# Kernel tuning notes

Measured on AMD Instinct MI355X. Metric: run time of the kernel, lower is better.

The kernel has to match this reference:

```python
import jax, jax.numpy as jnp
import numpy as np

B, S, DIM, HD = 4, 1024, 2048, 128
H = DIM // HD  # 16 heads
GN_EPS = 1e-3  # Keras GroupNormalization default epsilon


def setup_inputs() -> dict:
    key = jax.random.key(0)
    ks = jax.random.split(key, 8)
    x = jax.random.normal(ks[0], (B, S, DIM), dtype=jnp.float32)
    k = jax.random.normal(ks[1], (B, S, DIM), dtype=jnp.float32)
    v = jax.random.normal(ks[2], (B, S, DIM), dtype=jnp.float32)
    # One shared QKV projection weight per head (dict.fromkeys bug in source
    # makes Q, K, V use the SAME Dense layer). Keras Dense: y = x @ W, W:(in,out)
    Wh = jax.random.normal(ks[3], (H, HD, HD), dtype=jnp.float32) / np.sqrt(HD)
    wg_w = jax.random.normal(ks[4], (DIM, DIM), dtype=jnp.float32) / np.sqrt(DIM)
    wo_w = jax.random.normal(ks[5], (DIM, DIM), dtype=jnp.float32) / np.sqrt(DIM)
    gn_gamma = jnp.ones((DIM,), dtype=jnp.float32)
    gn_beta = jnp.zeros((DIM,), dtype=jnp.float32)
    return {"x": x, "k": k, "v": v, "Wh": Wh, "wg_w": wg_w, "wo_w": wo_w,
            "gn_gamma": gn_gamma, "gn_beta": gn_beta}


def _decay_masks(n_heads, seq_len):
    # Source: band_part(gamma**(i-j), 0, -1) then transpose ->
    # D[h, i, j] = gamma_h ** (j - i) for j <= i, else 0.
    gam = 1.0 - 2.0 ** (-5.0 - jnp.arange(n_heads, dtype=jnp.float32))  # (H,)
    idx = jnp.arange(seq_len, dtype=jnp.float32)
    expo = idx[None, :] - idx[:, None]               # (S,S): j - i
    D = jnp.where(expo[None, :, :] <= 0,
                  gam[:, None, None] ** expo[None, :, :], 0.0)  # (H,S,S)
    # TF: D /= reduce_sum(D, 1)**0.5 broadcasts row-sums along the COLUMN axis
    return D / jnp.sqrt(D.sum(axis=-1))[:, None, :]


def reference(x, k, v, Wh, wg_w, wo_w, gn_gamma, gn_beta):
    b, s, dim = x.shape
    h, hd, _ = Wh.shape
    # split last axis into contiguous per-head chunks
    xh = x.reshape(b, s, h, hd)
    kh = k.reshape(b, s, h, hd)
    vh = v.reshape(b, s, h, hd)
    # Q, K, V share the same per-head weight (faithful to dict.fromkeys)
    Q = jnp.einsum('bshd,hde->bshe', xh, Wh)
    K = jnp.einsum('bshd,hde->bshe', kh, Wh)
    V = jnp.einsum('bshd,hde->bshe', vh, Wh)
    scores = jnp.einsum('bshe,bthe->bhst', Q, K) / jnp.sqrt(jnp.float32(hd))
    Dn = _decay_masks(h, s)                          # (H,S,S)
    masked = scores * Dn[None, :, :, :]              # (B,H,S,S)
    # source reduces over axis 0 == BATCH, then abs, then clamp at 1
    A = jnp.maximum(jnp.abs(masked.sum(axis=0)), 1.0)  # (H,S,S)
    O = jnp.einsum('hst,bthe->bshe', A, V).reshape(b, s, dim)
    # GroupNormalization(groups=1): per-token layernorm over channels
    mu = O.mean(axis=-1, keepdims=True)
    var = O.var(axis=-1, keepdims=True)
    Y = (O - mu) / jnp.sqrt(var + GN_EPS) * gn_gamma + gn_beta
    W = jax.nn.relu(x @ wg_w)                        # gated branch
    return (W * Y) @ wo_w
```

## Files before the change

### kernel.cpp

```cpp
#include <hip/hip_runtime.h>
#include <math.h>

constexpr int Bc = 4, Sc = 1024, Dc = 2048, HDc = 128, Hc = 16;
constexpr int BSc = Bc * Sc;
constexpr int KQKc = Bc * HDc;
#define GN_EPS 1e-3f

typedef __bf16 bf16x8 __attribute__((ext_vector_type(8)));
typedef __bf16 bf16x4 __attribute__((ext_vector_type(4)));
typedef float f32x4 __attribute__((ext_vector_type(4)));

constexpr size_t OFF_Q   = 0;
constexpr size_t OFF_K   = OFF_Q + (size_t)Hc * Sc * KQKc / 2;
constexpr size_t OFF_VB  = OFF_K + (size_t)Hc * Sc * KQKc / 2;
constexpr size_t OFF_VT  = OFF_VB + (size_t)BSc * Dc / 2;
constexpr size_t OFF_A   = OFF_VT + (size_t)BSc * Dc / 2;
constexpr size_t OFF_O   = OFF_A + (size_t)Hc * Sc * Sc / 2;
constexpr size_t OFF_CT  = OFF_O + (size_t)BSc * Dc;
constexpr size_t OFF_PN  = OFF_CT + (size_t)Hc * Sc;
constexpr size_t OFF_XB  = OFF_PN + (size_t)Hc * Sc;
constexpr size_t OFF_WGT = OFF_XB + (size_t)BSc * Dc / 2;
constexpr size_t OFF_WOT = OFF_WGT + (size_t)Dc * Dc / 2;
constexpr size_t OFF_SUF = OFF_WOT + (size_t)Dc * Dc / 2;
constexpr size_t OFF_T   = OFF_SUF + (size_t)64 * 9 * HDc;
constexpr size_t OFF_WHT = OFF_T + (size_t)64 * 8 * HDc;
constexpr size_t OFF_KB2 = OFF_A;
constexpr size_t OFF_VB2 = OFF_A + (size_t)BSc * Dc / 2;

#define GLOAD_LDS16(gp, lp)                                               \
  __builtin_amdgcn_global_load_lds(                                       \
      (const __attribute__((address_space(1))) void*)(gp),                \
      (__attribute__((address_space(3))) void*)(lp), 16, 0, 0)


__global__ __launch_bounds__(256) void k_tables(float* __restrict__ ct,
                                                float* __restrict__ pn) {
  int idx = blockIdx.x * 256 + threadIdx.x;
  int h = idx >> 10, t = idx & 1023;
  double gamma = 1.0 - exp2(-(double)(5 + h));
  double l2g = log2(gamma);
  double r = 1.0 / gamma;
  double rowsum = (exp2(-(double)(t + 1) * l2g) - 1.0) / (r - 1.0);
  ct[idx] = (float)(exp2((double)t * l2g) / sqrt(rowsum));
  pn[idx] = (float)exp2(-(double)t * l2g);
}

__global__ __launch_bounds__(256) void k_cast8(const float* __restrict__ src,
                                               __bf16* __restrict__ dst) {
  size_t i = ((size_t)blockIdx.x * 256 + threadIdx.x) * 8;
  float4 a = *(const float4*)(src + i);
  float4 b = *(const float4*)(src + i + 4);
  bf16x8 o;
  o[0] = (__bf16)a.x; o[1] = (__bf16)a.y; o[2] = (__bf16)a.z; o[3] = (__bf16)a.w;
  o[4] = (__bf16)b.x; o[5] = (__bf16)b.y; o[6] = (__bf16)b.z; o[7] = (__bf16)b.w;
  *(bf16x8*)(dst + i) = o;
}

__global__ __launch_bounds__(256) void k_castT(const float* __restrict__ src,
                                               __bf16* __restrict__ dst) {
  __shared__ float t[32][33];
  const int bx = blockIdx.x, by = blockIdx.y;
  const int tid = threadIdx.x;
  const int lx = tid & 31, ly = tid >> 5;
  #pragma unroll
  for (int r = 0; r < 32; r += 8)
    t[ly + r][lx] = src[(size_t)(by * 32 + ly + r) * Dc + bx * 32 + lx];
  __syncthreads();
  #pragma unroll
  for (int r = 0; r < 32; r += 8)
    dst[(size_t)(bx * 32 + ly + r) * Dc + by * 32 + lx] = (__bf16)t[lx][ly + r];
}

__global__ __launch_bounds__(256) void k_whT(const float* __restrict__ Wh,
                                             __bf16* __restrict__ WhT) {
  __shared__ float t[32][33];
  const int h = blockIdx.z;
  const int d0 = blockIdx.x * 32, e0 = blockIdx.y * 32;
  const int tid = threadIdx.x;
  const int lx = tid & 31, ly = tid >> 5;
  #pragma unroll
  for (int r = 0; r < 32; r += 8)
    t[ly + r][lx] = Wh[(size_t)h * HDc * HDc + (d0 + ly + r) * HDc + e0 + lx];
  __syncthreads();
  #pragma unroll
  for (int r = 0; r < 32; r += 8)
    WhT[(size_t)h * HDc * HDc + (e0 + ly + r) * HDc + d0 + lx] =
        (__bf16)t[lx][ly + r];
}

__global__ __launch_bounds__(512) void k_projm(const __bf16* __restrict__ Xb,
                                               const __bf16* __restrict__ Kb2,
                                               const __bf16* __restrict__ Vb2,
                                               const __bf16* __restrict__ WhT,
                                               __bf16* __restrict__ Qo,
                                               __bf16* __restrict__ Ko,
                                               __bf16* __restrict__ Vo) {
  const int r0 = blockIdx.x * 128;
  const int h = blockIdx.y;
  const int z = blockIdx.z;
  const __bf16* src = (z == 0) ? Xb : (z == 1) ? Kb2 : Vb2;
  __shared__ __bf16 As[128 * 32];
  __shared__ __bf16 Bs[128 * 32];
  const int tid = threadIdx.x;
  const int wave = tid >> 6, lane = tid & 63;
  const int wm = (wave >> 2) * 64, wn = (wave & 3) * 32;
  const int grow = wave * 16 + (lane >> 2);
  const int gkb = ((lane & 3) ^ ((lane >> 3) & 3)) * 8;
  const int rl = lane & 15, kq = lane >> 4;
  const int sw8 = (kq ^ ((rl >> 1) & 3)) * 8;
  const int cha = wm >> 4, chb = wn >> 4;
  const __bf16* wb = WhT + (size_t)h * HDc * HDc;
  f32x4 acc[4][2] = {{}};
  for (int k0 = 0; k0 < HDc; k0 += 32) {
    GLOAD_LDS16(src + (size_t)(r0 + grow) * Dc + h * HDc + k0 + gkb,
                As + wave * 512);
    GLOAD_LDS16(wb + (size_t)grow * HDc + k0 + gkb, Bs + wave * 512);
    __syncthreads();
    bf16x8 a[4], b[2];
    #pragma unroll
    for (int i = 0; i < 4; ++i)
      a[i] = *(const bf16x8*)&As[(cha + i) * 512 + rl * 32 + sw8];
    #pragma unroll
    for (int j = 0; j < 2; ++j)
      b[j] = *(const bf16x8*)&Bs[(chb + j) * 512 + rl * 32 + sw8];
    #pragma unroll
    for (int i = 0; i < 4; ++i)
      #pragma unroll
      for (int j = 0; j < 2; ++j)
        acc[i][j] = __builtin_amdgcn_mfma_f32_16x16x32_bf16(a[i], b[j],
                                                            acc[i][j], 0, 0, 0);
    __syncthreads();
  }
  #pragma unroll
  for (int i = 0; i < 4; ++i) {
    #pragma unroll
    for (int j = 0; j < 2; ++j) {
      const int col = wn + j * 16 + rl;
      #pragma unroll
      for (int r = 0; r < 4; ++r) {
        const int row = r0 + wm + i * 16 + kq * 4 + r;
        const __bf16 v = (__bf16)acc[i][j][r];
        if (z == 2) {
          Vo[(size_t)row * Dc + h * HDc + col] = v;
        } else {
          const int s = row & 1023, bb = row >> 10;
          __bf16* dst = (z == 0) ? Qo : Ko;
          dst[((size_t)(h * Sc + s) * Bc + bb) * HDc + col] = v;
        }
      }
    }
  }
}

__global__ __launch_bounds__(256) void k_vt(const __bf16* __restrict__ VB,
                                            __bf16* __restrict__ Vt) {
  __shared__ float tl[32][33];
  const int bh = blockIdx.z, bb = bh >> 4, h = bh & 15;
  const int t0 = blockIdx.x * 32, e0 = blockIdx.y * 32;
  const int tid = threadIdx.x;
  const int lx = tid & 31, ly = tid >> 5;
  #pragma unroll
  for (int r = 0; r < 32; r += 8)
    tl[ly + r][lx] =
        (float)VB[(size_t)(bb * Sc + t0 + ly + r) * Dc + h * HDc + e0 + lx];
  __syncthreads();
  #pragma unroll
  for (int r = 0; r < 32; r += 8)
    Vt[((size_t)bh * HDc + e0 + ly + r) * Sc + t0 + lx] = (__bf16)tl[lx][ly + r];
}

__global__ __launch_bounds__(256) void k_vsum(const __bf16* __restrict__ VB,
                                              float* __restrict__ T) {
  const int jj = blockIdx.x, bh = blockIdx.y;
  const int bb = bh >> 4, h = bh & 15;
  const int tid = threadIdx.x;
  const int tp = tid >> 7, e = tid & 127;
  const __bf16* base =
      VB + (size_t)(bb * Sc + jj * 128 + tp * 64) * Dc + h * HDc + e;
  float a0 = 0.f, a1 = 0.f, a2 = 0.f, a3 = 0.f;
  float a4 = 0.f, a5 = 0.f, a6 = 0.f, a7 = 0.f;
  for (int t = 0; t < 64; t += 8) {
    a0 += (float)base[(size_t)(t + 0) * Dc];
    a1 += (float)base[(size_t)(t + 1) * Dc];
    a2 += (float)base[(size_t)(t + 2) * Dc];
    a3 += (float)base[(size_t)(t + 3) * Dc];
    a4 += (float)base[(size_t)(t + 4) * Dc];
    a5 += (float)base[(size_t)(t + 5) * Dc];
    a6 += (float)base[(size_t)(t + 6) * Dc];
    a7 += (float)base[(size_t)(t + 7) * Dc];
  }
  const float s = ((a0 + a1) + (a2 + a3)) + ((a4 + a5) + (a6 + a7));
  __shared__ float red[2][128];
  red[tp][e] = s;
  __syncthreads();
  if (tp == 0)
    T[((size_t)bh * 8 + jj) * HDc + e] = red[0][e] + red[1][e];
}

__global__ __launch_bounds__(128) void k_vscan(const float* __restrict__ T,
                                               float* __restrict__ SufV) {
  const int bh = blockIdx.x;
  const int e = threadIdx.x;
  float acc = 0.f;
  SufV[((size_t)bh * 9 + 8) * HDc + e] = 0.f;
  for (int jj = 7; jj >= 1; --jj) {
    acc += T[((size_t)bh * 8 + jj) * HDc + e];
    SufV[((size_t)bh * 9 + jj) * HDc + e] = acc;
  }
}

__global__ __launch_bounds__(512) void k_ssm(const __bf16* __restrict__ Q,
                                             const __bf16* __restrict__ Kb,
                                             const float* __restrict__ ct,
                                             const float* __restrict__ pn,
                                             __bf16* __restrict__ A) {
  const int bx = blockIdx.x, by = blockIdx.y;
  if (bx > by) return;
  const int h = blockIdx.z;
  const int t0 = bx * 128, s0 = by * 128;
  const int tid = threadIdx.x;
  __bf16* Ah = A + (size_t)h * Sc * Sc;
  __shared__ __bf16 Qs[128 * 32];
  __shared__ __bf16 Ks[128 * 32];
  const int wave = tid >> 6, lane = tid & 63;
  const int wm = (wave >> 2) * 64, wn = (wave & 3) * 32;
  const int grow = wave * 16 + (lane >> 2);
  const int gkb = ((lane & 3) ^ ((lane >> 3) & 3)) * 8;
  const int rl = lane & 15, kq = lane >> 4;
  const int sw8 = (kq ^ ((rl >> 1) & 3)) * 8;
  const int cha = wm >> 4, chb = wn >> 4;
  f32x4 acc[4][2] = {{}};
  const __bf16* qbase = Q + (size_t)(h * Sc + s0) * KQKc;
  const __bf16* kbase = Kb + (size_t)(h * Sc + t0) * KQKc;
  for (int k0 = 0; k0 < KQKc; k0 += 32) {
    GLOAD_LDS16(qbase + (size_t)grow * KQKc + k0 + gkb, Qs + wave * 512);
    GLOAD_LDS16(kbase + (size_t)grow * KQKc + k0 + gkb, Ks + wave * 512);
    __syncthreads();
    bf16x8 a[4], b[2];
    #pragma unroll
    for (int i = 0; i < 4; ++i)
      a[i] = *(const bf16x8*)&Qs[(cha + i) * 512 + rl * 32 + sw8];
    #pragma unroll
    for (int j = 0; j < 2; ++j)
      b[j] = *(const bf16x8*)&Ks[(chb + j) * 512 + rl * 32 + sw8];
    #pragma unroll
    for (int i = 0; i < 4; ++i)
      #pragma unroll
      for (int j = 0; j < 2; ++j)
        acc[i][j] = __builtin_amdgcn_mfma_f32_16x16x32_bf16(a[i], b[j],
                                                            acc[i][j], 0, 0, 0);
    __syncthreads();
  }
  const float rs = 0.088388347648318447f;
  #pragma unroll
  for (int i = 0; i < 4; ++i) {
    #pragma unroll
    for (int j = 0; j < 2; ++j) {
      const int t = t0 + wn + j * 16 + rl;
      const float ctv = ct[h * Sc + t] * rs;
      #pragma unroll
      for (int r = 0; r < 4; ++r) {
        const int s = s0 + wm + i * 16 + kq * 4 + r;
        float v = 1.0f;
        if (t <= s) v = fmaxf(fabsf(ctv * pn[h * Sc + s] * acc[i][j][r]), 1.0f);
        Ah[(size_t)s * Sc + t] = (__bf16)v;
      }
    }
  }
}

__global__ __launch_bounds__(512) void k_avm(const __bf16* __restrict__ A,
                                             const __bf16* __restrict__ Vt,
                                             const float* __restrict__ SufV,
                                             float* __restrict__ O) {
  const int bh = blockIdx.z, bb = bh >> 4, h = bh & 15;
  const int itile = blockIdx.x;
  const int s0 = itile * 128;
  const int tid = threadIdx.x;
  __shared__ __bf16 As[128 * 32];
  __shared__ __bf16 Bs[128 * 32];
  const int wave = tid >> 6, lane = tid & 63;
  const int wm = (wave >> 2) * 64, wn = (wave & 3) * 32;
  const int grow = wave * 16 + (lane >> 2);
  const int gkb = ((lane & 3) ^ ((lane >> 3) & 3)) * 8;
  const int rl = lane & 15, kq = lane >> 4;
  const int sw8 = (kq ^ ((rl >> 1) & 3)) * 8;
  const int cha = wm >> 4, chb = wn >> 4;
  f32x4 acc[4][2] = {{}};
  const __bf16* abase = A + (size_t)(h * Sc + s0) * Sc;
  const __bf16* vbase = Vt + (size_t)bh * HDc * Sc;
  const int kmax = (itile + 1) * 128;
  for (int k0 = 0; k0 < kmax; k0 += 32) {
    GLOAD_LDS16(abase + (size_t)grow * Sc + k0 + gkb, As + wave * 512);
    GLOAD_LDS16(vbase + (size_t)grow * Sc + k0 + gkb, Bs + wave * 512);
    __syncthreads();
    bf16x8 a[4], b[2];
    #pragma unroll
    for (int i = 0; i < 4; ++i)
      a[i] = *(const bf16x8*)&As[(cha + i) * 512 + rl * 32 + sw8];
    #pragma unroll
    for (int j = 0; j < 2; ++j)
      b[j] = *(const bf16x8*)&Bs[(chb + j) * 512 + rl * 32 + sw8];
    #pragma unroll
    for (int i = 0; i < 4; ++i)
      #pragma unroll
      for (int j = 0; j < 2; ++j)
        acc[i][j] = __builtin_amdgcn_mfma_f32_16x16x32_bf16(a[i], b[j],
                                                            acc[i][j], 0, 0, 0);
    __syncthreads();
  }
  const float* sufr = SufV + ((size_t)bh * 9 + (itile + 1)) * HDc;
  #pragma unroll
  for (int i = 0; i < 4; ++i) {
    #pragma unroll
    for (int j = 0; j < 2; ++j) {
      const int e = wn + j * 16 + rl;
      const float sv = sufr[e];
      #pragma unroll
      for (int r = 0; r < 4; ++r) {
        const int s = s0 + wm + i * 16 + kq * 4 + r;
        O[(size_t)(bb * Sc + s) * Dc + h * HDc + e] = acc[i][j][r] + sv;
      }
    }
  }
}

__global__ __launch_bounds__(256) void k_gnorm(float* __restrict__ O,
                                               const float* __restrict__ gw,
                                               const float* __restrict__ bw) {
  const int r = blockIdx.x;
  const int tid = threadIdx.x;
  float* row = O + (size_t)r * Dc;
  const int c = tid * 4;
  float4 v0 = *(const float4*)(row + c);
  float4 v1 = *(const float4*)(row + c + 1024);
  __shared__ float red[256];
  __shared__ float sh_mu, sh_inv;
  red[tid] = v0.x + v0.y + v0.z + v0.w + v1.x + v1.y + v1.z + v1.w;
  __syncthreads();
  for (int st = 128; st > 0; st >>= 1) {
    if (tid < st) red[tid] += red[tid + st];
    __syncthreads();
  }
  if (tid == 0) sh_mu = red[0] * (1.0f / Dc);
  __syncthreads();
  const float mu = sh_mu;
  float d[8] = {v0.x - mu, v0.y - mu, v0.z - mu, v0.w - mu,
                v1.x - mu, v1.y - mu, v1.z - mu, v1.w - mu};
  float ssq = 0.f;
  #pragma unroll
  for (int i = 0; i < 8; ++i) ssq += d[i] * d[i];
  red[tid] = ssq;
  __syncthreads();
  for (int st = 128; st > 0; st >>= 1) {
    if (tid < st) red[tid] += red[tid + st];
    __syncthreads();
  }
  if (tid == 0) sh_inv = rsqrtf(red[0] * (1.0f / Dc) + GN_EPS);
  __syncthreads();
  const float inv = sh_inv;
  float4 g0 = *(const float4*)(gw + c), g1 = *(const float4*)(gw + c + 1024);
  float4 b0 = *(const float4*)(bw + c), b1 = *(const float4*)(bw + c + 1024);
  float4 o0, o1;
  o0.x = d[0] * inv * g0.x + b0.x; o0.y = d[1] * inv * g0.y + b0.y;
  o0.z = d[2] * inv * g0.z + b0.z; o0.w = d[3] * inv * g0.w + b0.w;
  o1.x = d[4] * inv * g1.x + b1.x; o1.y = d[5] * inv * g1.y + b1.y;
  o1.z = d[6] * inv * g1.z + b1.z; o1.w = d[7] * inv * g1.w + b1.w;
  *(float4*)(row + c) = o0;
  *(float4*)(row + c + 1024) = o1;
}

__global__ __launch_bounds__(512) void k_mgemm(const __bf16* __restrict__ Ab,
                                               const __bf16* __restrict__ Bt,
                                               const float* __restrict__ Y,
                                               __bf16* __restrict__ Gout,
                                               float* __restrict__ Fout,
                                               int mode) {
  __shared__ __bf16 As[128 * 32];
  __shared__ __bf16 Bs[128 * 32];
  const int tid = threadIdx.x;
  const int wave = tid >> 6, lane = tid & 63;
  const int r0 = blockIdx.y * 128, c0 = blockIdx.x * 128;
  const int wm = (wave >> 2) * 64, wn = (wave & 3) * 32;
  const int grow = wave * 16 + (lane >> 2);
  const int gkb = ((lane & 3) ^ ((lane >> 3) & 3)) * 8;
  const int rl = lane & 15, kq = lane >> 4;
  const int sw8 = (kq ^ ((rl >> 1) & 3)) * 8;
  const int cha = wm >> 4, chb = wn >> 4;
  f32x4 acc[4][2] = {{}};

  for (int k0 = 0; k0 < Dc; k0 += 32) {
    GLOAD_LDS16(Ab + (size_t)(r0 + grow) * Dc + k0 + gkb, As + wave * 512);
    GLOAD_LDS16(Bt + (size_t)(c0 + grow) * Dc + k0 + gkb, Bs + wave * 512);
    __syncthreads();
    bf16x8 a[4], b[2];
    #pragma unroll
    for (int i = 0; i < 4; ++i)
      a[i] = *(const bf16x8*)&As[(cha + i) * 512 + rl * 32 + sw8];
    #pragma unroll
    for (int j = 0; j < 2; ++j)
      b[j] = *(const bf16x8*)&Bs[(chb + j) * 512 + rl * 32 + sw8];
    #pragma unroll
    for (int i = 0; i < 4; ++i)
      #pragma unroll
      for (int j = 0; j < 2; ++j)
        acc[i][j] = __builtin_amdgcn_mfma_f32_16x16x32_bf16(a[i], b[j],
                                                            acc[i][j], 0, 0, 0);
    __syncthreads();
  }

  #pragma unroll
  for (int i = 0; i < 4; ++i) {
    #pragma unroll
    for (int j = 0; j < 2; ++j) {
      const int col = c0 + wn + j * 16 + rl;
      #pragma unroll
      for (int r = 0; r < 4; ++r) {
        const int row = r0 + wm + i * 16 + kq * 4 + r;
        const size_t idx = (size_t)row * Dc + col;
        float v = acc[i][j][r];
        if (mode == 0) {
          v = fmaxf(v, 0.f) * Y[idx];
          Gout[idx] = (__bf16)v;
        } else {
          Fout[idx] = v;
        }
      }
    }
  }
}

extern "C" void kernel_launch(void* const* d_in, const int* in_sizes, int n_in,
                              void* d_out, int out_size, void* d_ws, size_t ws_size,
                              hipStream_t stream) {
  const float* x  = (const float*)d_in[0];
  const float* k  = (const float*)d_in[1];
  const float* v  = (const float*)d_in[2];
  const float* Wh = (const float*)d_in[3];
  const float* wg = (const float*)d_in[4];
  const float* wo = (const float*)d_in[5];
  const float* gg = (const float*)d_in[6];
  const float* gb = (const float*)d_in[7];
  float* ws = (float*)d_ws;
  __bf16* Q   = (__bf16*)(ws + OFF_Q);
  __bf16* Kp  = (__bf16*)(ws + OFF_K);
  __bf16* VB  = (__bf16*)(ws + OFF_VB);
  __bf16* Vt  = (__bf16*)(ws + OFF_VT);
  __bf16* A   = (__bf16*)(ws + OFF_A);
  float*  O   = ws + OFF_O;
  float*  CT  = ws + OFF_CT;
  float*  PN  = ws + OFF_PN;
  __bf16* XB  = (__bf16*)(ws + OFF_XB);
  __bf16* WGT = (__bf16*)(ws + OFF_WGT);
  __bf16* WOT = (__bf16*)(ws + OFF_WOT);
  float*  SUF = ws + OFF_SUF;
  float*  TP  = ws + OFF_T;
  __bf16* WHT = (__bf16*)(ws + OFF_WHT);
  __bf16* KB2 = (__bf16*)(ws + OFF_KB2);
  __bf16* VB2 = (__bf16*)(ws + OFF_VB2);
  __bf16* G   = (__bf16*)(ws + OFF_Q);

  k_tables<<<Hc * Sc / 256, 256, 0, stream>>>(CT, PN);
  k_cast8<<<(BSc * Dc) / (256 * 8), 256, 0, stream>>>(x, XB);
  k_cast8<<<(BSc * Dc) / (256 * 8), 256, 0, stream>>>(k, KB2);
  k_cast8<<<(BSc * Dc) / (256 * 8), 256, 0, stream>>>(v, VB2);
  k_castT<<<dim3(Dc / 32, Dc / 32), 256, 0, stream>>>(wg, WGT);
  k_castT<<<dim3(Dc / 32, Dc / 32), 256, 0, stream>>>(wo, WOT);
  k_whT<<<dim3(4, 4, Hc), 256, 0, stream>>>(Wh, WHT);
  k_projm<<<dim3(BSc / 128, Hc, 3), 512, 0, stream>>>(XB, KB2, VB2, WHT,
                                                      Q, Kp, VB);
  k_vt<<<dim3(Sc / 32, HDc / 32, Bc * Hc), 256, 0, stream>>>(VB, Vt);
  k_vsum<<<dim3(8, Bc * Hc), 256, 0, stream>>>(VB, TP);
  k_vscan<<<Bc * Hc, 128, 0, stream>>>(TP, SUF);
  k_ssm<<<dim3(Sc / 128, Sc / 128, Hc), 512, 0, stream>>>(Q, Kp, CT, PN, A);
  k_avm<<<dim3(Sc / 128, 1, Bc * Hc), 512, 0, stream>>>(A, Vt, SUF, O);
  k_gnorm<<<BSc, 256, 0, stream>>>(O, gg, gb);
  k_mgemm<<<dim3(Dc / 128, BSc / 128), 512, 0, stream>>>(XB, WGT, O, G, nullptr, 0);
  k_mgemm<<<dim3(Dc / 128, BSc / 128), 512, 0, stream>>>(G, WOT, nullptr, nullptr,
                                                         (float*)d_out, 1);
}
```

Baseline: 398.8 us.

## Rewrite gated/output GEMM with 256x128 tiles and multi-buffered async LDS pipeline

Rewrites the two final 4096x2048x2048 GEMMs. Each block now computes a larger 256x128 tile with a 64-deep K step, held in triple-buffered A and double-buffered B in dynamic LDS. Global-to-LDS loads are issued two iterations ahead, and the MFMA phases are interleaved with explicit waitcnt and barriers, setprio hints, and a grid swizzle for cache locality. The aim is to hide global memory latency and raise data reuse per loaded byte. The cost is much more LDS per block, tighter occupancy, and manual wait counts that are fragile to get right.

```diff
diff --git a/kernel.cpp b/kernel.cpp
--- a/kernel.cpp
+++ b/kernel.cpp
@@ -370,55 +370,136 @@
   *(float4*)(row + c + 1024) = o1;
 }
 
-__global__ __launch_bounds__(512) void k_mgemm(const __bf16* __restrict__ Ab,
-                                               const __bf16* __restrict__ Bt,
-                                               const float* __restrict__ Y,
-                                               __bf16* __restrict__ Gout,
-                                               float* __restrict__ Fout,
-                                               int mode) {
-  __shared__ __bf16 As[128 * 32];
-  __shared__ __bf16 Bs[128 * 32];
+constexpr int NTK = Dc / 64;
+constexpr int ABUFE = 256 * 64;
+constexpr int BBUFE = 128 * 64;
+constexpr int MG_LDS = (3 * ABUFE + 2 * BBUFE) * 2;
+
+__global__ __launch_bounds__(512, 2) void k_mgemm(const __bf16* __restrict__ Ab,
+                                                  const __bf16* __restrict__ Bt,
+                                                  const float* __restrict__ Y,
+                                                  __bf16* __restrict__ Gout,
+                                                  float* __restrict__ Fout,
+                                                  int mode) {
+  extern __shared__ __bf16 lds[];
+  __bf16* As = lds;
+  __bf16* Bs = lds + 3 * ABUFE;
+  int wid = blockIdx.y * gridDim.x + blockIdx.x;
+  wid = (wid & 7) * 32 + (wid >> 3);
+  const int r0 = (wid >> 4) * 256;
+  const int c0 = (wid & 15) * 128;
   const int tid = threadIdx.x;
   const int wave = tid >> 6, lane = tid & 63;
-  const int r0 = blockIdx.y * 128, c0 = blockIdx.x * 128;
-  const int wm = (wave >> 2) * 64, wn = (wave & 3) * 32;
-  const int grow = wave * 16 + (lane >> 2);
-  const int gkb = ((lane & 3) ^ ((lane >> 3) & 3)) * 8;
+  const int wr = wave >> 1, wc = wave & 1;
+  const int lr = lane >> 2;
+  const int lkx = ((lane & 3) ^ ((lane >> 3) & 3)) * 8;
   const int rl = lane & 15, kq = lane >> 4;
-  const int sw8 = (kq ^ ((rl >> 1) & 3)) * 8;
-  const int cha = wm >> 4, chb = wn >> 4;
-  f32x4 acc[4][2] = {{}};
-
-  for (int k0 = 0; k0 < Dc; k0 += 32) {
-    GLOAD_LDS16(Ab + (size_t)(r0 + grow) * Dc + k0 + gkb, As + wave * 512);
-    GLOAD_LDS16(Bt + (size_t)(c0 + grow) * Dc + k0 + gkb, Bs + wave * 512);
-    __syncthreads();
-    bf16x8 a[4], b[2];
-    #pragma unroll
-    for (int i = 0; i < 4; ++i)
-      a[i] = *(const bf16x8*)&As[(cha + i) * 512 + rl * 32 + sw8];
-    #pragma unroll
-    for (int j = 0; j < 2; ++j)
-      b[j] = *(const bf16x8*)&Bs[(chb + j) * 512 + rl * 32 + sw8];
-    #pragma unroll
-    for (int i = 0; i < 4; ++i)
-      #pragma unroll
-      for (int j = 0; j < 2; ++j)
-        acc[i][j] = __builtin_amdgcn_mfma_f32_16x16x32_bf16(a[i], b[j],
-                                                            acc[i][j], 0, 0, 0);
-    __syncthreads();
-  }
-
-  #pragma unroll
-  for (int i = 0; i < 4; ++i) {
-    #pragma unroll
-    for (int j = 0; j < 2; ++j) {
-      const int col = c0 + wn + j * 16 + rl;
+  const int swo = rl * 32 + ((kq ^ ((rl >> 1) & 3)) * 8);
+  f32x4 acc[4][4] = {{}};
+
+#define STAGE_A_(i, kt, bsel) do {                                          \
+    const int ci_ = (i) * 8 + wave;                                         \
+    GLOAD_LDS16(Ab + (size_t)(r0 + (ci_ >> 1) * 16 + lr) * Dc               \
+                    + (kt) * 64 + (ci_ & 1) * 32 + lkx,                     \
+                As + (bsel) * ABUFE + ci_ * 512);                           \
+  } while (0)
+#define STAGE_B_(j, kt, bsel) do {                                          \
+    const int ci_ = (j) * 8 + wave;                                         \
+    GLOAD_LDS16(Bt + (size_t)(c0 + (ci_ >> 1) * 16 + lr) * Dc               \
+                    + (kt) * 64 + (ci_ & 1) * 32 + lkx,                     \
+                Bs + (bsel) * BBUFE + ci_ * 512);                           \
+  } while (0)
+
+  STAGE_A_(0, 0, 0); STAGE_A_(1, 0, 0); STAGE_A_(2, 0, 0); STAGE_A_(3, 0, 0);
+  STAGE_B_(0, 0, 0); STAGE_B_(1, 0, 0);
+  STAGE_A_(0, 1, 1); STAGE_A_(1, 1, 1); STAGE_A_(2, 1, 1); STAGE_A_(3, 1, 1);
+  STAGE_B_(0, 1, 1); STAGE_B_(1, 1, 1);
+  __builtin_amdgcn_sched_barrier(0);
+  asm volatile("s_waitcnt vmcnt(6)" ::: "memory");
+  __builtin_amdgcn_sched_barrier(0);
+  __builtin_amdgcn_s_barrier();
+
+  int cbA = 0;
+  for (int t = 0; t < NTK; ++t) {
+    const int sbA = (cbA + 2 >= 3) ? cbA - 1 : cbA + 2;
+    const int cbB = t & 1;
+    const __bf16* Ac = As + cbA * ABUFE;
+    const __bf16* Bc = Bs + cbB * BBUFE;
+    const bool st = (t + 2) < NTK;
+    bf16x8 a0[2][2], a1[2][2], b[4][2];
+    #pragma unroll
+    for (int m = 0; m < 2; ++m)
+      #pragma unroll
+      for (int kc = 0; kc < 2; ++kc)
+        a0[m][kc] = *(const bf16x8*)&Ac[((wr * 4 + m) * 2 + kc) * 512 + swo];
+    #pragma unroll
+    for (int n = 0; n < 4; ++n)
+      #pragma unroll
+      for (int kc = 0; kc < 2; ++kc)
+        b[n][kc] = *(const bf16x8*)&Bc[((wc * 4 + n) * 2 + kc) * 512 + swo];
+    if (st) {
+      STAGE_A_(0, t + 2, sbA); STAGE_A_(1, t + 2, sbA); STAGE_A_(2, t + 2, sbA);
+    }
+    __builtin_amdgcn_sched_barrier(0);
+    __builtin_amdgcn_s_barrier();
+    asm volatile("s_waitcnt lgkmcnt(0)" ::: "memory");
+    __builtin_amdgcn_sched_barrier(0);
+    __builtin_amdgcn_s_setprio(1);
+    #pragma unroll
+    for (int kc = 0; kc < 2; ++kc)
+      #pragma unroll
+      for (int m = 0; m < 2; ++m)
+        #pragma unroll
+        for (int n = 0; n < 4; ++n)
+          acc[m][n] = __builtin_amdgcn_mfma_f32_16x16x32_bf16(
+              a0[m][kc], b[n][kc], acc[m][n], 0, 0, 0);
+    __builtin_amdgcn_s_setprio(0);
+    __builtin_amdgcn_sched_barrier(0);
+    __builtin_amdgcn_s_barrier();
+    #pragma unroll
+    for (int m = 0; m < 2; ++m)
+      #pragma unroll
+      for (int kc = 0; kc < 2; ++kc)
+        a1[m][kc] = *(const bf16x8*)&Ac[((wr * 4 + 2 + m) * 2 + kc) * 512 + swo];
+    if (st) {
+      STAGE_A_(3, t + 2, sbA); STAGE_B_(0, t + 2, cbB); STAGE_B_(1, t + 2, cbB);
+    }
+    __builtin_amdgcn_sched_barrier(0);
+    if (st)
+      asm volatile("s_waitcnt vmcnt(6)" ::: "memory");
+    else if (t + 1 < NTK)
+      asm volatile("s_waitcnt vmcnt(0)" ::: "memory");
+    __builtin_amdgcn_sched_barrier(0);
+    __builtin_amdgcn_s_barrier();
+    asm volatile("s_waitcnt lgkmcnt(0)" ::: "memory");
+    __builtin_amdgcn_sched_barrier(0);
+    __builtin_amdgcn_s_setprio(1);
+    #pragma unroll
+    for (int kc = 0; kc < 2; ++kc)
+      #pragma unroll
+      for (int m = 0; m < 2; ++m)
+        #pragma unroll
+        for (int n = 0; n < 4; ++n)
+          acc[2 + m][n] = __builtin_amdgcn_mfma_f32_16x16x32_bf16(
+              a1[m][kc], b[n][kc], acc[2 + m][n], 0, 0, 0);
+    __builtin_amdgcn_s_setprio(0);
+    __builtin_amdgcn_sched_barrier(0);
+    __builtin_amdgcn_s_barrier();
+    cbA = (cbA + 1 >= 3) ? 0 : cbA + 1;
+  }
+#undef STAGE_A_
+#undef STAGE_B_
+
+  #pragma unroll
+  for (int mi = 0; mi < 4; ++mi) {
+    #pragma unroll
+    for (int nj = 0; nj < 4; ++nj) {
+      const int col = c0 + wc * 64 + nj * 16 + rl;
       #pragma unroll
       for (int r = 0; r < 4; ++r) {
-        const int row = r0 + wm + i * 16 + kq * 4 + r;
+        const int row = r0 + wr * 64 + mi * 16 + kq * 4 + r;
         const size_t idx = (size_t)row * Dc + col;
-        float v = acc[i][j][r];
+        float v = acc[mi][nj][r];
         if (mode == 0) {
           v = fmaxf(v, 0.f) * Y[idx];
           Gout[idx] = (__bf16)v;
@@ -460,6 +541,14 @@
   __bf16* VB2 = (__bf16*)(ws + OFF_VB2);
   __bf16* G   = (__bf16*)(ws + OFF_Q);
 
+  static bool attr_done = false;
+  if (!attr_done) {
+    (void)hipFuncSetAttribute((const void*)k_mgemm,
+                              hipFuncAttributeMaxDynamicSharedMemorySize,
+                              MG_LDS);
+    attr_done = true;
+  }
+
   k_tables<<<Hc * Sc / 256, 256, 0, stream>>>(CT, PN);
   k_cast8<<<(BSc * Dc) / (256 * 8), 256, 0, stream>>>(x, XB);
   k_cast8<<<(BSc * Dc) / (256 * 8), 256, 0, stream>>>(k, KB2);
@@ -475,7 +564,7 @@
   k_ssm<<<dim3(Sc / 128, Sc / 128, Hc), 512, 0, stream>>>(Q, Kp, CT, PN, A);
   k_avm<<<dim3(Sc / 128, 1, Bc * Hc), 512, 0, stream>>>(A, Vt, SUF, O);
   k_gnorm<<<BSc, 256, 0, stream>>>(O, gg, gb);
-  k_mgemm<<<dim3(Dc / 128, BSc / 128), 512, 0, stream>>>(XB, WGT, O, G, nullptr, 0);
-  k_mgemm<<<dim3(Dc / 128, BSc / 128), 512, 0, stream>>>(G, WOT, nullptr, nullptr,
-                                                         (float*)d_out, 1);
-}
+  k_mgemm<<<dim3(16, 16), 512, MG_LDS, stream>>>(XB, WGT, O, G, nullptr, 0);
+  k_mgemm<<<dim3(16, 16), 512, MG_LDS, stream>>>(G, WOT, nullptr, nullptr,
+                                                 (float*)d_out, 1);
+}
```

Result: faster. 385.6 us (-3.3%).
